# Optimization experiments

Hardware: AMD Instinct MI355X
Metric: run time of the kernel (lower is better)

## Reference

```python
import jax, jax.numpy as jnp
import numpy as np

L, B, IN, D = 1024, 32, 1024, 1024

def setup_inputs() -> dict:
    key = jax.random.key(0)
    k1, k2, k3 = jax.random.split(key, 3)
    sigma_w = (3.0 / IN) ** 0.5
    x = jax.random.normal(k1, (L, B, IN), dtype=jnp.float32)
    W = jax.random.uniform(k2, (IN, 4 * D), dtype=jnp.float32, minval=-sigma_w, maxval=sigma_w)
    V = jax.random.uniform(k3, (2 * D,), dtype=jnp.float32, minval=-(3.0 ** 0.5), maxval=3.0 ** 0.5)
    b = jnp.zeros((2 * D,), dtype=jnp.float32)
    c0 = jnp.zeros((B, D), dtype=jnp.float32)
    return {"x": x, "c0": c0, "W": W, "V": V, "b": b}

def reference(x, c0, W, V, b):
    # U: [L, B, D, 4] -- single big GEMM, matches input.view(-1,in).mm(W)
    U = jnp.einsum('lbi,ij->lbj', x, W).reshape(L, B, D, 4)
    v_f, v_r = V[:D], V[D:]
    b_f, b_r = b[:D], b[D:]

    def step(c_prev, u):
        # u: [B, D, 4]
        f_t = jax.nn.sigmoid(u[..., 1] + c_prev * v_f + b_f)
        r_t = jax.nn.sigmoid(u[..., 2] + c_prev * v_r + b_r)
        c_t = u[..., 0] + (c_prev - u[..., 0]) * f_t
        h_t = (jnp.tanh(c_t) - u[..., 3]) * r_t + u[..., 3]
        return c_t, h_t

    c_last, h = jax.lax.scan(step, c0, U)
    return h, c_last
```

## Files before the change

### kernel.cpp

```cpp
#include <hip/hip_runtime.h>
#include <stdint.h>

#define L_   1024
#define B_   32
#define IN_  1024
#define D_   1024
#define M_   (L_ * B_)
#define N4_  (4 * D_)
#define K_   IN_

#define L2E      1.4426950408889634f
#define TWO_L2E  2.8853900817779268f

typedef _Float16 f16x8 __attribute__((ext_vector_type(8)));
typedef float    f32x4 __attribute__((ext_vector_type(4)));

#define GLB(p) (const __attribute__((address_space(1))) void*)(p)
#define LDSP(p) (__attribute__((address_space(3))) void*)(p)

__device__ __forceinline__ unsigned short f2h(float f) {
  _Float16 h = (_Float16)f;
  return __builtin_bit_cast(unsigned short, h);
}
__device__ __forceinline__ float h2f(unsigned short b) {
  return (float)__builtin_bit_cast(_Float16, b);
}

__global__ void cvt_x(const float* __restrict__ x, unsigned short* __restrict__ xh) {
  int i = (blockIdx.x * 256 + threadIdx.x) * 4;
  float4 v = *(const float4*)(x + i);
  ushort4 o;
  o.x = f2h(v.x); o.y = f2h(v.y); o.z = f2h(v.z); o.w = f2h(v.w);
  *(ushort4*)(xh + i) = o;
}

__global__ void cvt_wt(const float* __restrict__ W, unsigned short* __restrict__ Wt) {
  __shared__ float t[32][33];
  int tx = threadIdx.x, ty = threadIdx.y;
  int x0 = blockIdx.x * 32, y0 = blockIdx.y * 32;
  t[ty][tx] = W[(size_t)(y0 + ty) * N4_ + x0 + tx];
  __syncthreads();
  int n = x0 + ty;
  int g = n & 3;
  float s = (g == 1 || g == 2) ? L2E : 1.0f;
  Wt[(size_t)n * K_ + y0 + tx] = f2h(t[tx][ty] * s);
}

__global__ __launch_bounds__(256) void gemm_u(const unsigned short* __restrict__ A,
                                              const unsigned short* __restrict__ Bt,
                                              unsigned short* __restrict__ U) {
  __shared__ unsigned short As[128 * 32];
  __shared__ unsigned short Bs[128 * 32];

  const int tid  = threadIdx.x;
  const int wave = tid >> 6;
  const int lane = tid & 63;
  const int l15  = lane & 15;
  const int quad = lane >> 4;
  const int wm   = wave & 1;
  const int wn   = wave >> 1;
  const int m0   = blockIdx.y * 128;
  const int n0   = blockIdx.x * 128;

  const int srow = lane >> 2;
  const int scol = (lane & 3) * 8;

  f32x4 acc[4][4];
#pragma unroll
  for (int i = 0; i < 4; i++)
#pragma unroll
    for (int j = 0; j < 4; j++) acc[i][j] = (f32x4){0.f, 0.f, 0.f, 0.f};

  for (int k0 = 0; k0 < K_; k0 += 32) {
#pragma unroll
    for (int c = 0; c < 2; c++) {
      const int chunk = wave * 2 + c;
      const int row   = chunk * 16 + srow;
      const unsigned short* ga = A  + (size_t)(m0 + row) * K_ + k0 + scol;
      const unsigned short* gb = Bt + (size_t)(n0 + row) * K_ + k0 + scol;
      __builtin_amdgcn_global_load_lds(GLB(ga), LDSP(As + chunk * 512), 16, 0, 0);
      __builtin_amdgcn_global_load_lds(GLB(gb), LDSP(Bs + chunk * 512), 16, 0, 0);
    }
    __syncthreads();

    const f16x8* Af = (const f16x8*)As;
    const f16x8* Bf = (const f16x8*)Bs;
    f16x8 a[4], b[4];
#pragma unroll
    for (int mi = 0; mi < 4; mi++) a[mi] = Af[(wm * 64 + mi * 16 + l15) * 4 + quad];
#pragma unroll
    for (int ni = 0; ni < 4; ni++) b[ni] = Bf[(wn * 64 + ni * 16 + l15) * 4 + quad];
#pragma unroll
    for (int mi = 0; mi < 4; mi++)
#pragma unroll
      for (int ni = 0; ni < 4; ni++)
        acc[mi][ni] = __builtin_amdgcn_mfma_f32_16x16x32_f16(a[mi], b[ni], acc[mi][ni], 0, 0, 0);
    __syncthreads();
  }

#pragma unroll
  for (int mi = 0; mi < 4; mi++) {
#pragma unroll
    for (int ni = 0; ni < 4; ni++) {
      const int row = m0 + wm * 64 + mi * 16 + quad * 4;
      const int col = n0 + wn * 64 + ni * 16 + l15;
#pragma unroll
      for (int i = 0; i < 4; i++)
        U[(size_t)(row + i) * N4_ + col] = f2h(acc[mi][ni][i]);
    }
  }
}

__global__ __launch_bounds__(64) void scan_kernel(const unsigned short* __restrict__ U,
                                                  const float* __restrict__ c0,
                                                  const float* __restrict__ V,
                                                  const float* __restrict__ bias,
                                                  float* __restrict__ out) {
  const int t = blockIdx.x * 64 + threadIdx.x;
  const int d = t & (D_ - 1);
  float c = c0[t];
  const float vfp = V[d] * L2E, vrp = V[D_ + d] * L2E;
  const float bfp = bias[d] * L2E, brp = bias[D_ + d] * L2E;
  const uint2* Up = (const uint2*)U;

  constexpr int PF = 16;
  uint2 buf[PF];
#pragma unroll
  for (int j = 0; j < PF; j++) buf[j] = Up[(size_t)j * 32768 + t];

#define SRU_STEP(u, l)                                                          \
  {                                                                             \
    const float u0 = h2f((unsigned short)((u).x & 0xffffu));                    \
    const float u1 = h2f((unsigned short)((u).x >> 16));        \
    const float u2 = h2f((unsigned short)((u).y & 0xffffu));    \
    const float u3 = h2f((unsigned short)((u).y >> 16));                        \
    const float pf = fmaf(c, vfp, u1 + bfp);                                    \
    const float pr = fmaf(c, vrp, u2 + brp);                                    \
    const float f  = __builtin_amdgcn_rcpf(1.f + __builtin_amdgcn_exp2f(-pf));  \
    const float r  = __builtin_amdgcn_rcpf(1.f + __builtin_amdgcn_exp2f(-pr));  \
    c = fmaf(c - u0, f, u0);                                                    \
    const float q  = __builtin_amdgcn_exp2f(c * TWO_L2E);                       \
    const float th = fmaf(-2.f, __builtin_amdgcn_rcpf(1.f + q), 1.f);           \
    const float h  = fmaf(th - u3, r, u3);                                      \
    __builtin_nontemporal_store(h, out + (size_t)(l) * 32768 + t);              \
  }

#pragma unroll 1
  for (int l0 = 0; l0 < L_ - PF; l0 += PF) {
#pragma unroll
    for (int j = 0; j < PF; j++) {
      uint2 u = buf[j];
      buf[j] = Up[(size_t)(l0 + j + PF) * 32768 + t];
      SRU_STEP(u, l0 + j);
    }
  }
#pragma unroll
  for (int j = 0; j < PF; j++) {
    uint2 u = buf[j];
    SRU_STEP(u, L_ - PF + j);
  }
#undef SRU_STEP

  out[(size_t)L_ * 32768 + t] = c;
}

extern "C" void kernel_launch(void* const* d_in, const int* in_sizes, int n_in,
                              void* d_out, int out_size, void* d_ws, size_t ws_size,
                              hipStream_t stream) {
  const float* x    = (const float*)d_in[0];
  const float* c0   = (const float*)d_in[1];
  const float* W    = (const float*)d_in[2];
  const float* V    = (const float*)d_in[3];
  const float* bias = (const float*)d_in[4];
  float* out = (float*)d_out;

  uint8_t* ws = (uint8_t*)d_ws;
  unsigned short* Xh = (unsigned short*)ws;
  unsigned short* Wt = (unsigned short*)(ws + ((size_t)64 << 20));
  unsigned short* U  = (unsigned short*)(ws + ((size_t)72 << 20));

  cvt_x<<<(M_ * K_) / 1024, 256, 0, stream>>>(x, Xh);
  cvt_wt<<<dim3(N4_ / 32, K_ / 32), dim3(32, 32), 0, stream>>>(W, Wt);
  gemm_u<<<dim3(N4_ / 128, M_ / 128), 256, 0, stream>>>(Xh, Wt, U);
  scan_kernel<<<(B_ * D_) / 64, 64, 0, stream>>>(U, c0, V, bias, out);
}
```

Measured before the change: 667.2 us.

## Rewrite GEMM as 256x256 tile, 8-wave, multi-stage pipelined kernel with swizzled LDS

Replaces the simple 128x128 single-buffered GEMM with a 256x256-tile, 512-thread kernel. It double-buffers 64-wide K tiles in 128KB of LDS using async global-to-LDS loads interleaved with MFMA phases, XOR-swizzled LDS offsets, s_setprio around MFMA bursts, and a block-index swizzle for L2 locality. The goal is to hide global load latency and raise MFMA utilization in the dominant GEMM. The cost is heavy LDS use, which limits occupancy, plus a complex hand-coded waitcnt and barrier schedule that could be fragile.

```diff
diff --git a/kernel.cpp b/kernel.cpp
--- a/kernel.cpp
+++ b/kernel.cpp
@@ -46,69 +46,116 @@
   Wt[(size_t)n * K_ + y0 + tx] = f2h(t[tx][ty] * s);
 }
 
-__global__ __launch_bounds__(256) void gemm_u(const unsigned short* __restrict__ A,
-                                              const unsigned short* __restrict__ Bt,
-                                              unsigned short* __restrict__ U) {
-  __shared__ unsigned short As[128 * 32];
-  __shared__ unsigned short Bs[128 * 32];
+
+#define BARRIER() do { __builtin_amdgcn_sched_barrier(0); __builtin_amdgcn_s_barrier(); \
+                       __builtin_amdgcn_sched_barrier(0); } while (0)
+#define VMW8 asm volatile("s_waitcnt vmcnt(8)" ::: "memory")
+#define SBAR0 __builtin_amdgcn_sched_barrier(0)
+
+__device__ __forceinline__ void stage_half(const unsigned short* __restrict__ g,
+                                           unsigned short* __restrict__ half_,
+                                           int rowbase, int ktile, int kk,
+                                           int wave, int srow, int skel) {
+  const int kt = ktile < 15 ? ktile : 15;
+  const unsigned short* g0 =
+      g + (size_t)(rowbase + wave * 32 + srow) * K_ + kt * 64 + kk * 32 + skel;
+  __builtin_amdgcn_global_load_lds(GLB(g0), LDSP(half_ + wave * 1024), 16, 0, 0);
+  __builtin_amdgcn_global_load_lds(GLB(g0 + (size_t)16 * K_),
+                                   LDSP(half_ + wave * 1024 + 512), 16, 0, 0);
+}
+
+__global__ __launch_bounds__(512, 2) void gemm_u(const unsigned short* __restrict__ A,
+                                                 const unsigned short* __restrict__ Bt,
+                                                 unsigned short* __restrict__ U) {
+  __shared__ unsigned short lds[65536];
 
   const int tid  = threadIdx.x;
   const int wave = tid >> 6;
   const int lane = tid & 63;
   const int l15  = lane & 15;
   const int quad = lane >> 4;
-  const int wm   = wave & 1;
-  const int wn   = wave >> 1;
-  const int m0   = blockIdx.y * 128;
-  const int n0   = blockIdx.x * 128;
+  const int wm   = wave >> 2;
+  const int wn   = wave & 3;
+
+  const int bid = blockIdx.x;
+  const int swz = (bid & 7) * 256 + (bid >> 3);
+  const int n0  = (swz & 15) * 256;
+  const int m0  = (swz >> 4) * 256;
 
   const int srow = lane >> 2;
-  const int scol = (lane & 3) * 8;
-
-  f32x4 acc[4][4];
-#pragma unroll
-  for (int i = 0; i < 4; i++)
+  const int skel = ((lane & 3) * 8) ^ ((lane >= 32) ? 16 : 0);
+
+  const int roff = (l15 * 32 + quad * 8) ^ ((l15 >= 8) ? 16 : 0);
+
+#define HA(s, h) (lds + ((s)*2 + (h)) * 8192)
+#define HB(s, h) (lds + 32768 + ((s)*2 + (h)) * 8192)
+
+  f32x4 acc[8][4];
+#pragma unroll
+  for (int i = 0; i < 8; i++)
 #pragma unroll
     for (int j = 0; j < 4; j++) acc[i][j] = (f32x4){0.f, 0.f, 0.f, 0.f};
 
-  for (int k0 = 0; k0 < K_; k0 += 32) {
-#pragma unroll
-    for (int c = 0; c < 2; c++) {
-      const int chunk = wave * 2 + c;
-      const int row   = chunk * 16 + srow;
-      const unsigned short* ga = A  + (size_t)(m0 + row) * K_ + k0 + scol;
-      const unsigned short* gb = Bt + (size_t)(n0 + row) * K_ + k0 + scol;
-      __builtin_amdgcn_global_load_lds(GLB(ga), LDSP(As + chunk * 512), 16, 0, 0);
-      __builtin_amdgcn_global_load_lds(GLB(gb), LDSP(Bs + chunk * 512), 16, 0, 0);
-    }
-    __syncthreads();
-
-    const f16x8* Af = (const f16x8*)As;
-    const f16x8* Bf = (const f16x8*)Bs;
-    f16x8 a[4], b[4];
-#pragma unroll
-    for (int mi = 0; mi < 4; mi++) a[mi] = Af[(wm * 64 + mi * 16 + l15) * 4 + quad];
-#pragma unroll
-    for (int ni = 0; ni < 4; ni++) b[ni] = Bf[(wn * 64 + ni * 16 + l15) * 4 + quad];
-#pragma unroll
-    for (int mi = 0; mi < 4; mi++)
-#pragma unroll
-      for (int ni = 0; ni < 4; ni++)
-        acc[mi][ni] = __builtin_amdgcn_mfma_f32_16x16x32_f16(a[mi], b[ni], acc[mi][ni], 0, 0, 0);
-    __syncthreads();
-  }
-
-#pragma unroll
-  for (int mi = 0; mi < 4; mi++) {
-#pragma unroll
-    for (int ni = 0; ni < 4; ni++) {
-      const int row = m0 + wm * 64 + mi * 16 + quad * 4;
+  stage_half(A,  HA(0, 0), m0, 0, 0, wave, srow, skel); SBAR0;
+  stage_half(Bt, HB(0, 0), n0, 0, 0, wave, srow, skel); SBAR0;
+  stage_half(A,  HA(0, 1), m0, 0, 1, wave, srow, skel); SBAR0;
+  stage_half(Bt, HB(0, 1), n0, 0, 1, wave, srow, skel); SBAR0;
+  stage_half(A,  HA(1, 0), m0, 1, 0, wave, srow, skel); SBAR0;
+  stage_half(Bt, HB(1, 0), n0, 1, 0, wave, srow, skel); SBAR0;
+  VMW8;
+  BARRIER();
+
+  f16x8 afr[4], bfr[4];
+
+#define PHASE(S, KK, MH, GMAT, LHALF, ROWB, KT, KH, DO_VMW)                        \
+  {                                                                                \
+    const unsigned short* ha = HA(S, KK);                                          \
+    if ((MH) == 0) {                                                               \
+      const unsigned short* hb = HB(S, KK);                                        \
+      _Pragma("unroll") for (int ni = 0; ni < 4; ++ni)                             \
+          bfr[ni] = *(const f16x8*)(hb + (wn * 4 + ni) * 512 + roff);              \
+    }                                                                              \
+    _Pragma("unroll") for (int mi = 0; mi < 4; ++mi)                               \
+        afr[mi] = *(const f16x8*)(ha + (wm * 8 + (MH)*4 + mi) * 512 + roff);       \
+    stage_half(GMAT, LHALF, ROWB, KT, KH, wave, srow, skel);                       \
+    BARRIER();                                                                     \
+    __builtin_amdgcn_s_setprio(1);                                                 \
+    _Pragma("unroll") for (int mi = 0; mi < 4; ++mi)                               \
+        _Pragma("unroll") for (int ni = 0; ni < 4; ++ni)                           \
+            acc[(MH)*4 + mi][ni] = __builtin_amdgcn_mfma_f32_16x16x32_f16(         \
+                afr[mi], bfr[ni], acc[(MH)*4 + mi][ni], 0, 0, 0);                  \
+    __builtin_amdgcn_s_setprio(0);                                                 \
+    if (DO_VMW) VMW8;                                                              \
+    BARRIER();                                                                     \
+  }
+
+#pragma unroll 1
+  for (int it = 0; it < 8; ++it) {
+    const int t1 = 2 * it + 1, t2 = 2 * it + 2, t3 = 2 * it + 3;
+    PHASE(0, 0, 0, A,  HA(1, 1), m0, t1, 1, 0)
+    PHASE(0, 0, 1, Bt, HB(1, 1), n0, t1, 1, 1)
+    PHASE(0, 1, 0, A,  HA(0, 0), m0, t2, 0, 0)
+    PHASE(0, 1, 1, Bt, HB(0, 0), n0, t2, 0, 1)
+    PHASE(1, 0, 0, A,  HA(0, 1), m0, t2, 1, 0)
+    PHASE(1, 0, 1, Bt, HB(0, 1), n0, t2, 1, 1)
+    PHASE(1, 1, 0, A,  HA(1, 0), m0, t3, 0, 0)
+    PHASE(1, 1, 1, Bt, HB(1, 0), n0, t3, 0, 1)
+  }
+#undef PHASE
+
+#pragma unroll
+  for (int mi = 0; mi < 8; ++mi) {
+#pragma unroll
+    for (int ni = 0; ni < 4; ++ni) {
+      const int row = m0 + wm * 128 + mi * 16 + quad * 4;
       const int col = n0 + wn * 64 + ni * 16 + l15;
 #pragma unroll
-      for (int i = 0; i < 4; i++)
+      for (int i = 0; i < 4; ++i)
         U[(size_t)(row + i) * N4_ + col] = f2h(acc[mi][ni][i]);
     }
   }
+#undef HA
+#undef HB
 }
 
 __global__ __launch_bounds__(64) void scan_kernel(const unsigned short* __restrict__ U,
@@ -181,6 +228,6 @@
 
   cvt_x<<<(M_ * K_) / 1024, 256, 0, stream>>>(x, Xh);
   cvt_wt<<<dim3(N4_ / 32, K_ / 32), dim3(32, 32), 0, stream>>>(W, Wt);
-  gemm_u<<<dim3(N4_ / 128, M_ / 128), 256, 0, stream>>>(Xh, Wt, U);
+  gemm_u<<<2048, 512, 0, stream>>>(Xh, Wt, U);
   scan_kernel<<<(B_ * D_) / 64, 64, 0, stream>>>(U, c0, V, bias, out);
 }
```

After: 625.9 us. -6.2%, faster.
